# Kernel optimization log

Hardware: AMD Instinct MI355X
Metric: run time of the kernel (lower is better)

The kernel has to match this reference:

```python
import jax, jax.numpy as jnp
import numpy as np

B, S, C, H, D = 4, 2048, 512, 8, 64
EPS = 1e-5
SCALE = D ** -0.5


def layer_norm(x, w, b):
    m = jnp.mean(x, axis=-1, keepdims=True)
    v = jnp.var(x, axis=-1, keepdims=True)
    return (x - m) * jax.lax.rsqrt(v + EPS) * w + b


def setup_inputs() -> dict:
    key = jax.random.key(0)
    ks = jax.random.split(key, 7)
    s = 0.02
    return {
        "x": jax.random.normal(ks[0], (B, S, C), jnp.float32),
        "Wq": jax.random.normal(ks[1], (C, H * D), jnp.float32) * s,
        "Wk": jax.random.normal(ks[2], (C, H * D), jnp.float32) * s,
        "Wv": jax.random.normal(ks[3], (C, H * D), jnp.float32) * s,
        "Wo": jax.random.normal(ks[4], (H * D, C), jnp.float32) * s,
        "ln1_w": jnp.ones((C,), jnp.float32), "ln1_b": jnp.zeros((C,), jnp.float32),
        "ff_ln1_w": jnp.ones((C,), jnp.float32), "ff_ln1_b": jnp.zeros((C,), jnp.float32),
        "ff_w1": jax.random.normal(ks[5], (C, C), jnp.float32) * s, "ff_b1": jnp.zeros((C,), jnp.float32),
        "ff_ln2_w": jnp.ones((C,), jnp.float32), "ff_ln2_b": jnp.zeros((C,), jnp.float32),
        "ff_w2": jax.random.normal(ks[6], (C, C), jnp.float32) * s, "ff_b2": jnp.zeros((C,), jnp.float32),
        "ln2_w": jnp.ones((C,), jnp.float32), "ln2_b": jnp.zeros((C,), jnp.float32),
    }


def causal_attention(x, Wq, Wk, Wv, Wo):
    # Mathematically identical to the bucketed memory-efficient attention:
    # online-softmax bucketing changes compute order, not the result.
    q = (x @ Wq).reshape(B, S, H, D).transpose(0, 2, 1, 3)  # [B,H,S,D]
    k = (x @ Wk).reshape(B, S, H, D).transpose(0, 2, 1, 3)
    v = (x @ Wv).reshape(B, S, H, D).transpose(0, 2, 1, 3)
    scores = jnp.einsum('bhqd,bhkd->bhqk', q, k) * SCALE  # [B,H,S,S]
    causal = jnp.tril(jnp.ones((S, S), bool))
    scores = jnp.where(causal, scores, jnp.finfo(scores.dtype).min)
    attn = jax.nn.softmax(scores, axis=-1)
    out = jnp.einsum('bhqk,bhkd->bhqd', attn, v)
    out = out.transpose(0, 2, 1, 3).reshape(B, S, H * D)
    return out @ Wo


def reference(x, Wq, Wk, Wv, Wo, ln1_w, ln1_b, ff_ln1_w, ff_ln1_b, ff_w1, ff_b1,
              ff_ln2_w, ff_ln2_b, ff_w2, ff_b2, ln2_w, ln2_b):
    a = causal_attention(x, Wq, Wk, Wv, Wo)
    x_ln = layer_norm(a + x, ln1_w, ln1_b)
    h = layer_norm(x_ln, ff_ln1_w, ff_ln1_b) @ ff_w1 + ff_b1
    h = layer_norm(h, ff_ln2_w, ff_ln2_b) @ ff_w2 + ff_b2
    return layer_norm(h + x_ln, ln2_w, ln2_b)
```

## Files before the change

kernel.cpp:

```cpp
#include <hip/hip_runtime.h>

#define B_ 4
#define S_ 2048
#define C_ 512
#define H_ 8
#define D_ 64
#define M_ 8192

typedef short s8v __attribute__((ext_vector_type(8)));
typedef short s4v __attribute__((ext_vector_type(4)));
typedef float f4v __attribute__((ext_vector_type(4)));
typedef unsigned short u16;
typedef unsigned int u32;

__device__ __forceinline__ u16 f2b(float f) {
    u32 u = __builtin_bit_cast(u32, f);
    u = u + 0x7fffu + ((u >> 16) & 1u);
    return (u16)(u >> 16);
}

__device__ __forceinline__ void b2f8(const s8v v, float* f) {
    #pragma unroll
    for (int k = 0; k < 8; ++k)
        f[k] = __builtin_bit_cast(float, (u32)(u16)v[k] << 16);
}

__device__ __forceinline__ void gl2lds16(const void* g, void* l) {
    __builtin_amdgcn_global_load_lds(
        (const __attribute__((address_space(1))) void*)g,
        (__attribute__((address_space(3))) void*)l, 16, 0, 0);
}

__global__ __launch_bounds__(256) void prep_k(const float* __restrict__ x,
                                              u16* __restrict__ xb,
                                              const float* __restrict__ s0,
                                              const float* __restrict__ s1,
                                              const float* __restrict__ s2,
                                              const float* __restrict__ s3,
                                              const float* __restrict__ s4,
                                              const float* __restrict__ s5,
                                              u16* __restrict__ d0,
                                              u16* __restrict__ d1,
                                              u16* __restrict__ d2,
                                              u16* __restrict__ d3,
                                              u16* __restrict__ d4,
                                              u16* __restrict__ d5)
{
    __shared__ float t[32][33];
    const int bx = blockIdx.x;
    if (bx < 4096) {
        const int i = (bx * 256 + (int)threadIdx.x) * 4;
        const float4 v = *(const float4*)&x[i];
        ushort4 o;
        o.x = f2b(v.x); o.y = f2b(v.y); o.z = f2b(v.z); o.w = f2b(v.w);
        *(ushort4*)&xb[i] = o;
        return;
    }
    const int tb = bx - 4096;
    const int z = tb >> 8, rem = tb & 255;
    const float* W; u16* Wt;
    switch (z) {
        case 0: W = s0; Wt = d0; break;
        case 1: W = s1; Wt = d1; break;
        case 2: W = s2; Wt = d2; break;
        case 3: W = s3; Wt = d3; break;
        case 4: W = s4; Wt = d4; break;
        default: W = s5; Wt = d5; break;
    }
    const int tx = threadIdx.x & 31, ty = threadIdx.x >> 5;
    const int n0 = (rem & 15) * 32, k0 = (rem >> 4) * 32;
    #pragma unroll
    for (int i = 0; i < 4; ++i)
        t[ty + i * 8][tx] = W[(size_t)(k0 + ty + i * 8) * C_ + n0 + tx];
    __syncthreads();
    #pragma unroll
    for (int i = 0; i < 4; ++i)
        Wt[(size_t)(n0 + ty + i * 8) * C_ + k0 + tx] = f2b(t[tx][ty + i * 8]);
}

template <bool OB>
__global__ __launch_bounds__(256) void gemm_k(const u16* __restrict__ A,
                                              const u16* __restrict__ Bt,
                                              const float* __restrict__ bias,
                                              void* __restrict__ outv)
{
    __shared__ u16 As[2][4][16][32];
    __shared__ u16 Bs[2][4][16][32];
    const int tid = threadIdx.x;
    const int lane = tid & 63, w = tid >> 6;
    const int q4 = lane >> 4, l16 = lane & 15;
    const int wr = w >> 1, wc = w & 1;
    const int bm = blockIdx.y * 64, bn = blockIdx.x * 64;
    const int lr = lane >> 2, lc = (lane & 3) * 8;

    f4v acc[2][2];
    #pragma unroll
    for (int i = 0; i < 2; ++i)
        #pragma unroll
        for (int j = 0; j < 2; ++j) acc[i][j] = (f4v){0.f, 0.f, 0.f, 0.f};

    gl2lds16(A  + (size_t)(bm + w * 16 + lr) * C_ + lc, (char*)As + w * 1024);
    gl2lds16(Bt + (size_t)(bn + w * 16 + lr) * C_ + lc, (char*)Bs + w * 1024);

    for (int kt = 0; kt < 16; ++kt) {
        __syncthreads();
        const int buf = kt & 1;
        if (kt < 15) {
            const int nb = buf ^ 1, k0 = (kt + 1) * 32;
            gl2lds16(A  + (size_t)(bm + w * 16 + lr) * C_ + k0 + lc,
                     (char*)As + nb * 4096 + w * 1024);
            gl2lds16(Bt + (size_t)(bn + w * 16 + lr) * C_ + k0 + lc,
                     (char*)Bs + nb * 4096 + w * 1024);
        }
        s8v a[2], bfr[2];
        #pragma unroll
        for (int i = 0; i < 2; ++i) {
            const int row = wr * 32 + i * 16 + l16;
            a[i] = *(const s8v*)&As[buf][row >> 4][row & 15][q4 * 8];
        }
        #pragma unroll
        for (int j = 0; j < 2; ++j) {
            const int row = wc * 32 + j * 16 + l16;
            bfr[j] = *(const s8v*)&Bs[buf][row >> 4][row & 15][q4 * 8];
        }
        #pragma unroll
        for (int i = 0; i < 2; ++i)
            #pragma unroll
            for (int j = 0; j < 2; ++j)
                acc[i][j] = __builtin_amdgcn_mfma_f32_16x16x32_bf16(a[i], bfr[j], acc[i][j], 0, 0, 0);
    }

    #pragma unroll
    for (int j = 0; j < 2; ++j) {
        const int n = bn + wc * 32 + j * 16 + l16;
        const float bj = bias ? bias[n] : 0.0f;
        #pragma unroll
        for (int i = 0; i < 2; ++i) {
            const int m = bm + wr * 32 + i * 16 + q4 * 4;
            #pragma unroll
            for (int reg = 0; reg < 4; ++reg) {
                const float vv = acc[i][j][reg] + bj;
                if constexpr (OB) ((u16*)outv)[(size_t)(m + reg) * C_ + n] = f2b(vv);
                else              ((float*)outv)[(size_t)(m + reg) * C_ + n] = vv;
            }
        }
    }
}

__global__ __launch_bounds__(256) void qkv_k(const u16* __restrict__ A,
                                             const u16* __restrict__ Wq,
                                             const u16* __restrict__ Wk,
                                             const u16* __restrict__ Wv,
                                             u16* __restrict__ oq,
                                             u16* __restrict__ ok,
                                             u16* __restrict__ ovt)
{
    __shared__ u16 As[2][4][16][32];
    __shared__ u16 Bs[2][4][16][32];
    const int tid = threadIdx.x;
    const int lane = tid & 63, w = tid >> 6;
    const int q4 = lane >> 4, l16 = lane & 15;
    const int wr = w >> 1, wc = w & 1;
    const int nt = blockIdx.x, which = nt >> 3;
    const u16* Bt = which == 0 ? Wq : (which == 1 ? Wk : Wv);
    const int bm = blockIdx.y * 64, bn = (nt & 7) * 64;
    const int lr = lane >> 2, lc = (lane & 3) * 8;

    f4v acc[2][2];
    #pragma unroll
    for (int i = 0; i < 2; ++i)
        #pragma unroll
        for (int j = 0; j < 2; ++j) acc[i][j] = (f4v){0.f, 0.f, 0.f, 0.f};

    gl2lds16(A  + (size_t)(bm + w * 16 + lr) * C_ + lc, (char*)As + w * 1024);
    gl2lds16(Bt + (size_t)(bn + w * 16 + lr) * C_ + lc, (char*)Bs + w * 1024);

    for (int kt = 0; kt < 16; ++kt) {
        __syncthreads();
        const int buf = kt & 1;
        if (kt < 15) {
            const int nb = buf ^ 1, k0 = (kt + 1) * 32;
            gl2lds16(A  + (size_t)(bm + w * 16 + lr) * C_ + k0 + lc,
                     (char*)As + nb * 4096 + w * 1024);
            gl2lds16(Bt + (size_t)(bn + w * 16 + lr) * C_ + k0 + lc,
                     (char*)Bs + nb * 4096 + w * 1024);
        }
        s8v a[2], bfr[2];
        #pragma unroll
        for (int i = 0; i < 2; ++i) {
            const int row = wr * 32 + i * 16 + l16;
            a[i] = *(const s8v*)&As[buf][row >> 4][row & 15][q4 * 8];
        }
        #pragma unroll
        for (int j = 0; j < 2; ++j) {
            const int row = wc * 32 + j * 16 + l16;
            bfr[j] = *(const s8v*)&Bs[buf][row >> 4][row & 15][q4 * 8];
        }
        #pragma unroll
        for (int i = 0; i < 2; ++i)
            #pragma unroll
            for (int j = 0; j < 2; ++j)
                acc[i][j] = __builtin_amdgcn_mfma_f32_16x16x32_bf16(a[i], bfr[j], acc[i][j], 0, 0, 0);
    }

    if (which == 0) {
        #pragma unroll
        for (int j = 0; j < 2; ++j) {
            const int n = bn + wc * 32 + j * 16 + l16;
            #pragma unroll
            for (int i = 0; i < 2; ++i) {
                const int m = bm + wr * 32 + i * 16 + q4 * 4;
                #pragma unroll
                for (int reg = 0; reg < 4; ++reg)
                    oq[(size_t)(m + reg) * C_ + n] = f2b(acc[i][j][reg]);
            }
        }
    } else if (which == 1) {
        #pragma unroll
        for (int j = 0; j < 2; ++j) {
            const int n = bn + wc * 32 + j * 16 + l16;
            const int nswz = (n & ~31) | ((((n >> 3) & 3) ^ q4) << 3) | (n & 7);
            #pragma unroll
            for (int i = 0; i < 2; ++i) {
                const int m = bm + wr * 32 + i * 16 + q4 * 4;
                #pragma unroll
                for (int reg = 0; reg < 4; ++reg)
                    ok[(size_t)(m + reg) * C_ + nswz] = f2b(acc[i][j][reg]);
            }
        }
    } else {
        const int bglob = bm >> 11;
        const int sbase = bm & (S_ - 1);
        #pragma unroll
        for (int j = 0; j < 2; ++j) {
            const int n = bn + wc * 32 + j * 16 + l16;
            const int h = n >> 6, d = n & 63;
            u16* vrow = ovt + ((size_t)(bglob * H_ + h) * D_ + d) * S_;
            const int xw = d & 7;
            #pragma unroll
            for (int i = 0; i < 2; ++i) {
                const int s = sbase + wr * 32 + i * 16 + q4 * 4;
                const int pg = ((s & 31) >> 2) ^ xw;
                s4v pv;
                #pragma unroll
                for (int reg = 0; reg < 4; ++reg) pv[reg] = (short)f2b(acc[i][j][reg]);
                *(s4v*)&vrow[(s & ~31) + (pg << 2)] = pv;
            }
        }
    }
}

__global__ __launch_bounds__(256) void ln2xb_k(const u16* __restrict__ in,
                                               const float* __restrict__ res,
                                               const float* __restrict__ w1,
                                               const float* __restrict__ b1,
                                               const float* __restrict__ w2,
                                               const float* __restrict__ b2,
                                               u16* __restrict__ out1,
                                               u16* __restrict__ out2)
{
    const int lane = threadIdx.x & 63;
    const int row  = blockIdx.x * 4 + (threadIdx.x >> 6);
    const size_t off = (size_t)row * C_ + lane * 8;
    float v[8];
    b2f8(*(const s8v*)&in[off], v);
    {
        const float4 r0 = *(const float4*)&res[off];
        const float4 r1 = *(const float4*)&res[off + 4];
        v[0] += r0.x; v[1] += r0.y; v[2] += r0.z; v[3] += r0.w;
        v[4] += r1.x; v[5] += r1.y; v[6] += r1.z; v[7] += r1.w;
    }
    float s = 0.f, ss = 0.f;
    #pragma unroll
    for (int k = 0; k < 8; ++k) { s += v[k]; ss += v[k] * v[k]; }
    #pragma unroll
    for (int o = 32; o >= 1; o >>= 1) { s += __shfl_xor(s, o); ss += __shfl_xor(ss, o); }
    float mean = s * (1.0f / C_);
    float rstd = rsqrtf(ss * (1.0f / C_) - mean * mean + 1e-5f);

    const float4 wA0 = *(const float4*)&w1[lane * 8];
    const float4 wA1 = *(const float4*)&w1[lane * 8 + 4];
    const float4 bA0 = *(const float4*)&b1[lane * 8];
    const float4 bA1 = *(const float4*)&b1[lane * 8 + 4];
    const float wA[8] = {wA0.x, wA0.y, wA0.z, wA0.w, wA1.x, wA1.y, wA1.z, wA1.w};
    const float bA[8] = {bA0.x, bA0.y, bA0.z, bA0.w, bA1.x, bA1.y, bA1.z, bA1.w};
    float y[8];
    s8v o1;
    #pragma unroll
    for (int k = 0; k < 8; ++k) {
        y[k] = (v[k] - mean) * rstd * wA[k] + bA[k];
        o1[k] = (short)f2b(y[k]);
    }
    *(s8v*)&out1[off] = o1;

    s = 0.f; ss = 0.f;
    #pragma unroll
    for (int k = 0; k < 8; ++k) { s += y[k]; ss += y[k] * y[k]; }
    #pragma unroll
    for (int o = 32; o >= 1; o >>= 1) { s += __shfl_xor(s, o); ss += __shfl_xor(ss, o); }
    mean = s * (1.0f / C_);
    rstd = rsqrtf(ss * (1.0f / C_) - mean * mean + 1e-5f);

    const float4 wB0 = *(const float4*)&w2[lane * 8];
    const float4 wB1 = *(const float4*)&w2[lane * 8 + 4];
    const float4 bB0 = *(const float4*)&b2[lane * 8];
    const float4 bB1 = *(const float4*)&b2[lane * 8 + 4];
    const float wB[8] = {wB0.x, wB0.y, wB0.z, wB0.w, wB1.x, wB1.y, wB1.z, wB1.w};
    const float bB[8] = {bB0.x, bB0.y, bB0.z, bB0.w, bB1.x, bB1.y, bB1.z, bB1.w};
    s8v o2;
    #pragma unroll
    for (int k = 0; k < 8; ++k)
        o2[k] = (short)f2b((y[k] - mean) * rstd * wB[k] + bB[k]);
    *(s8v*)&out2[off] = o2;
}

__global__ __launch_bounds__(256) void lnb_k(const u16* __restrict__ in,
                                             const float* __restrict__ w,
                                             const float* __restrict__ bb,
                                             u16* __restrict__ out)
{
    const int lane = threadIdx.x & 63;
    const int row  = blockIdx.x * 4 + (threadIdx.x >> 6);
    const size_t off = (size_t)row * C_ + lane * 8;
    float v[8];
    b2f8(*(const s8v*)&in[off], v);
    float s = 0.f, ss = 0.f;
    #pragma unroll
    for (int k = 0; k < 8; ++k) { s += v[k]; ss += v[k] * v[k]; }
    #pragma unroll
    for (int o = 32; o >= 1; o >>= 1) { s += __shfl_xor(s, o); ss += __shfl_xor(ss, o); }
    const float mean = s * (1.0f / C_);
    const float rstd = rsqrtf(ss * (1.0f / C_) - mean * mean + 1e-5f);
    const float4 w0 = *(const float4*)&w[lane * 8];
    const float4 w1 = *(const float4*)&w[lane * 8 + 4];
    const float4 b0 = *(const float4*)&bb[lane * 8];
    const float4 b1 = *(const float4*)&bb[lane * 8 + 4];
    const float wv[8] = {w0.x, w0.y, w0.z, w0.w, w1.x, w1.y, w1.z, w1.w};
    const float bv[8] = {b0.x, b0.y, b0.z, b0.w, b1.x, b1.y, b1.z, b1.w};
    s8v o;
    #pragma unroll
    for (int k = 0; k < 8; ++k)
        o[k] = (short)f2b((v[k] - mean) * rstd * wv[k] + bv[k]);
    *(s8v*)&out[off] = o;
}

__global__ __launch_bounds__(256) void lnfin_k(const u16* __restrict__ in,
                                               const u16* __restrict__ res,
                                               const float* __restrict__ w,
                                               const float* __restrict__ bb,
                                               float* __restrict__ out)
{
    const int lane = threadIdx.x & 63;
    const int row  = blockIdx.x * 4 + (threadIdx.x >> 6);
    const size_t off = (size_t)row * C_ + lane * 8;
    float v[8], r[8];
    b2f8(*(const s8v*)&in[off], v);
    b2f8(*(const s8v*)&res[off], r);
    #pragma unroll
    for (int k = 0; k < 8; ++k) v[k] += r[k];
    float s = 0.f, ss = 0.f;
    #pragma unroll
    for (int k = 0; k < 8; ++k) { s += v[k]; ss += v[k] * v[k]; }
    #pragma unroll
    for (int o = 32; o >= 1; o >>= 1) { s += __shfl_xor(s, o); ss += __shfl_xor(ss, o); }
    const float mean = s * (1.0f / C_);
    const float rstd = rsqrtf(ss * (1.0f / C_) - mean * mean + 1e-5f);
    const float4 w0 = *(const float4*)&w[lane * 8];
    const float4 w1 = *(const float4*)&w[lane * 8 + 4];
    const float4 b0 = *(const float4*)&bb[lane * 8];
    const float4 b1 = *(const float4*)&bb[lane * 8 + 4];
    const float wv[8] = {w0.x, w0.y, w0.z, w0.w, w1.x, w1.y, w1.z, w1.w};
    const float bv[8] = {b0.x, b0.y, b0.z, b0.w, b1.x, b1.y, b1.z, b1.w};
    float4 o0, o1;
    o0.x = (v[0] - mean) * rstd * wv[0] + bv[0];
    o0.y = (v[1] - mean) * rstd * wv[1] + bv[1];
    o0.z = (v[2] - mean) * rstd * wv[2] + bv[2];
    o0.w = (v[3] - mean) * rstd * wv[3] + bv[3];
    o1.x = (v[4] - mean) * rstd * wv[4] + bv[4];
    o1.y = (v[5] - mean) * rstd * wv[5] + bv[5];
    o1.z = (v[6] - mean) * rstd * wv[6] + bv[6];
    o1.w = (v[7] - mean) * rstd * wv[7] + bv[7];
    *(float4*)&out[off]     = o0;
    *(float4*)&out[off + 4] = o1;
}

__global__ __launch_bounds__(256) void attn_k(const u16* __restrict__ Q,
                                              const u16* __restrict__ K,
                                              const u16* __restrict__ Vt,
                                              u16* __restrict__ O)
{
    __shared__ u16 Ks[2][2][64][32];
    __shared__ u16 Vs[2][2][64][32];
    const int tid = threadIdx.x;
    const int lane = tid & 63, w = tid >> 6;
    const int q4 = lane >> 4, l16 = lane & 15;
    const int h = blockIdx.y, b = blockIdx.z;
    const int qb = 31 - (int)blockIdx.x;
    const size_t base  = ((size_t)b * S_) * C_ + h * D_;
    const size_t basev = ((size_t)(b * H_ + h)) * D_ * S_;
    const int lr = lane >> 2, lc = (lane & 3) * 8;
    const int kq = (q4 ^ ((l16 >> 2) & 3)) * 8;

    s8v qf[2];
    #pragma unroll
    for (int kh = 0; kh < 2; ++kh)
        qf[kh] = *(const s8v*)&Q[base + (size_t)(qb * 64 + w * 16 + l16) * C_ + kh * 32 + q4 * 8];

    #pragma unroll
    for (int r = 0; r < 2; ++r) {
        const int seg = r * 4 + w;
        const int row = (seg & 3) * 16 + lr;
        const int kh = seg >> 2;
        gl2lds16(K  + base  + (size_t)row * C_ + kh * 32 + lc, (char*)Ks + seg * 1024);
        gl2lds16(Vt + basev + (size_t)row * S_ + kh * 32 + lc, (char*)Vs + seg * 1024);
    }

    f4v o[4];
    float lp[4] = {0.f, 0.f, 0.f, 0.f};
    #pragma unroll
    for (int j = 0; j < 4; ++j) o[j] = (f4v){0.f, 0.f, 0.f, 0.f};

    const int qrow = w * 16 + l16;
    for (int kb = 0; kb <= qb; ++kb) {
        __syncthreads();
        const int buf = kb & 1;
        if (kb < qb) {
            const int nb = buf ^ 1, kn = kb + 1;
            #pragma unroll
            for (int r = 0; r < 2; ++r) {
                const int seg = r * 4 + w;
                const int row = (seg & 3) * 16 + lr;
                const int kh = seg >> 2;
                gl2lds16(K  + base  + (size_t)(kn * 64 + row) * C_ + kh * 32 + lc,
                         (char*)Ks + nb * 8192 + seg * 1024);
                gl2lds16(Vt + basev + (size_t)row * S_ + kn * 64 + kh * 32 + lc,
                         (char*)Vs + nb * 8192 + seg * 1024);
            }
        }

        f4v sc[4];
        #pragma unroll
        for (int j = 0; j < 4; ++j) sc[j] = (f4v){0.f, 0.f, 0.f, 0.f};
        #pragma unroll
        for (int kh = 0; kh < 2; ++kh) {
            #pragma unroll
            for (int j = 0; j < 4; ++j) {
                const s8v kf = *(const s8v*)&Ks[buf][kh][j * 16 + l16][kq];
                sc[j] = __builtin_amdgcn_mfma_f32_16x16x32_bf16(kf, qf[kh], sc[j], 0, 0, 0);
            }
        }

        s4v pa[4];
        if (kb == qb) {
            #pragma unroll
            for (int j = 0; j < 4; ++j) {
                float ps = 0.0f;
                #pragma unroll
                for (int reg = 0; reg < 4; ++reg) {
                    float t = fmaf(sc[j][reg], 0.18033688011112043f, -11.541560327111707f);
                    if ((j * 16 + q4 * 4 + reg) > qrow) t = -128.0f;
                    const float p = exp2f(t);
                    ps += p;
                    pa[j][reg] = (short)(__builtin_bit_cast(u32, p) >> 16);
                }
                lp[j] += ps;
            }
        } else {
            #pragma unroll
            for (int j = 0; j < 4; ++j) {
                float ps = 0.0f;
                #pragma unroll
                for (int reg = 0; reg < 4; ++reg) {
                    const float p = exp2f(fmaf(sc[j][reg], 0.18033688011112043f,
                                               -11.541560327111707f));
                    ps += p;
                    pa[j][reg] = (short)(__builtin_bit_cast(u32, p) >> 16);
                }
                lp[j] += ps;
            }
        }

        #pragma unroll
        for (int c = 0; c < 4; ++c) {
            const int gh = (((c & 1) * 4 + q4) ^ (l16 & 7)) * 4;
            #pragma unroll
            for (int dj = 0; dj < 4; ++dj) {
                const s4v vb = *(const s4v*)&Vs[buf][c >> 1][dj * 16 + l16][gh];
                o[dj] = __builtin_amdgcn_mfma_f32_16x16x16bf16_1k(pa[c], vb, o[dj], 0, 0, 0);
            }
        }
    }

    float lt = (lp[0] + lp[1]) + (lp[2] + lp[3]);
    lt += __shfl_xor(lt, 16);
    lt += __shfl_xor(lt, 32);
    #pragma unroll
    for (int reg = 0; reg < 4; ++reg) {
        const float inv = 1.0f / __shfl(lt, q4 * 4 + reg);
        const size_t rowoff = base + (size_t)(qb * 64 + w * 16 + q4 * 4 + reg) * C_;
        #pragma unroll
        for (int dj = 0; dj < 4; ++dj)
            O[rowoff + dj * 16 + l16] = f2b(o[dj][reg] * inv);
    }
}

extern "C" void kernel_launch(void* const* d_in, const int* in_sizes, int n_in,
                              void* d_out, int out_size, void* d_ws, size_t ws_size,
                              hipStream_t stream)
{
    const float* x       = (const float*)d_in[0];
    const float* Wq      = (const float*)d_in[1];
    const float* Wk      = (const float*)d_in[2];
    const float* Wv      = (const float*)d_in[3];
    const float* Wo      = (const float*)d_in[4];
    const float* ln1_w   = (const float*)d_in[5];
    const float* ln1_b   = (const float*)d_in[6];
    const float* ffln1_w = (const float*)d_in[7];
    const float* ffln1_b = (const float*)d_in[8];
    const float* ff_w1   = (const float*)d_in[9];
    const float* ff_b1   = (const float*)d_in[10];
    const float* ffln2_w = (const float*)d_in[11];
    const float* ffln2_b = (const float*)d_in[12];
    const float* ff_w2   = (const float*)d_in[13];
    const float* ff_b2   = (const float*)d_in[14];
    const float* ln2_w   = (const float*)d_in[15];
    const float* ln2_b   = (const float*)d_in[16];
    float* out = (float*)d_out;

    const size_t MC = (size_t)M_ * C_;
    const size_t WW = (size_t)C_ * C_;
    u16* xb   = (u16*)d_ws;
    u16* WqT  = xb + MC;
    u16* WkT  = WqT + WW;
    u16* WvT  = WkT + WW;
    u16* WoT  = WvT + WW;
    u16* W1T  = WoT + WW;
    u16* W2T  = W1T + WW;
    u16* qbuf = W2T + WW;
    u16* kbuf = qbuf + MC;
    u16* vbuf = kbuf + MC;
    u16* vtbuf= vbuf + MC;
    u16*  abuf = xb;
    u16*  tf   = qbuf;
    u16*  xln  = vbuf;

    const dim3 gg(C_ / 64, M_ / 64);
    const dim3 gq(24, M_ / 64);
    const dim3 ga(32, H_, B_);
    const int  gl = M_ / 4;

    prep_k<<<5632, 256, 0, stream>>>(x, xb, Wq, Wk, Wv, Wo, ff_w1, ff_w2,
                                     WqT, WkT, WvT, WoT, W1T, W2T);

    qkv_k<<<gq, 256, 0, stream>>>(xb, WqT, WkT, WvT, qbuf, kbuf, vtbuf);
    attn_k<<<ga, 256, 0, stream>>>(qbuf, kbuf, vtbuf, abuf);

    gemm_k<true><<<gg, 256, 0, stream>>>(abuf, WoT, nullptr, tf);
    ln2xb_k<<<gl, 256, 0, stream>>>(tf, x, ln1_w, ln1_b, ffln1_w, ffln1_b,
                                    xln, xb);
    gemm_k<true><<<gg, 256, 0, stream>>>(xb, W1T, ff_b1, tf);
    lnb_k<<<gl, 256, 0, stream>>>(tf, ffln2_w, ffln2_b, xb);
    gemm_k<true><<<gg, 256, 0, stream>>>(xb, W2T, ff_b2, tf);
    lnfin_k<<<gl, 256, 0, stream>>>(tf, xln, ln2_w, ln2_b, out);
}
```

Before: 262.7 us.

## Enlarge GEMM tiles to 128x64 with K=64 stages and XOR-swizzled LDS

Both the generic GEMM and the fused QKV projection now use 128x64 output tiles with 64-wide K stages instead of 64x64 tiles with 32-wide K stages. Each wave computes a 64x32 sub-tile (4x2 MFMAs) and does two MFMA k-steps per barrier. The LDS layout is row-major with an XOR swizzle to avoid bank conflicts. The grid is transposed so consecutive blocks walk along M and share the same weight tile. This cuts the number of barriers and global loads per MFMA, at the cost of more LDS and registers per block and fewer blocks overall.

Result: faster. 242.7 us (-7.6%).

```diff
diff --git a/kernel.cpp b/kernel.cpp
--- a/kernel.cpp
+++ b/kernel.cpp
@@ -84,50 +84,58 @@
                                               const float* __restrict__ bias,
                                               void* __restrict__ outv)
 {
-    __shared__ u16 As[2][4][16][32];
-    __shared__ u16 Bs[2][4][16][32];
+    __shared__ u16 As[2][128][64];
+    __shared__ u16 Bs[2][64][64];
     const int tid = threadIdx.x;
     const int lane = tid & 63, w = tid >> 6;
     const int q4 = lane >> 4, l16 = lane & 15;
     const int wr = w >> 1, wc = w & 1;
-    const int bm = blockIdx.y * 64, bn = blockIdx.x * 64;
-    const int lr = lane >> 2, lc = (lane & 3) * 8;
-
-    f4v acc[2][2];
-    #pragma unroll
-    for (int i = 0; i < 2; ++i)
+    const int bm = blockIdx.x * 128, bn = blockIdx.y * 64;
+    const int sr8  = lane >> 3;
+    const int scol = ((lane & 7) ^ sr8) * 8;
+
+    f4v acc[4][2];
+    #pragma unroll
+    for (int i = 0; i < 4; ++i)
         #pragma unroll
         for (int j = 0; j < 2; ++j) acc[i][j] = (f4v){0.f, 0.f, 0.f, 0.f};
 
-    gl2lds16(A  + (size_t)(bm + w * 16 + lr) * C_ + lc, (char*)As + w * 1024);
-    gl2lds16(Bt + (size_t)(bn + w * 16 + lr) * C_ + lc, (char*)Bs + w * 1024);
-
-    for (int kt = 0; kt < 16; ++kt) {
+    const u16* Ab = A  + (size_t)bm * C_;
+    const u16* Bb = Bt + (size_t)bn * C_;
+
+    auto stage = [&](int bf, int kt) {
+        const int k0 = kt * 64;
+        #pragma unroll
+        for (int t = 0; t < 4; ++t)
+            gl2lds16(Ab + (size_t)(w * 32 + t * 8 + sr8) * C_ + k0 + scol,
+                     (char*)As + bf * 16384 + (w * 32 + t * 8) * 128);
+        #pragma unroll
+        for (int t = 0; t < 2; ++t)
+            gl2lds16(Bb + (size_t)(w * 16 + t * 8 + sr8) * C_ + k0 + scol,
+                     (char*)Bs + bf * 8192 + (w * 16 + t * 8) * 128);
+    };
+
+    stage(0, 0);
+    for (int kt = 0; kt < 8; ++kt) {
         __syncthreads();
-        const int buf = kt & 1;
-        if (kt < 15) {
-            const int nb = buf ^ 1, k0 = (kt + 1) * 32;
-            gl2lds16(A  + (size_t)(bm + w * 16 + lr) * C_ + k0 + lc,
-                     (char*)As + nb * 4096 + w * 1024);
-            gl2lds16(Bt + (size_t)(bn + w * 16 + lr) * C_ + k0 + lc,
-                     (char*)Bs + nb * 4096 + w * 1024);
-        }
-        s8v a[2], bfr[2];
-        #pragma unroll
-        for (int i = 0; i < 2; ++i) {
-            const int row = wr * 32 + i * 16 + l16;
-            a[i] = *(const s8v*)&As[buf][row >> 4][row & 15][q4 * 8];
-        }
-        #pragma unroll
-        for (int j = 0; j < 2; ++j) {
-            const int row = wc * 32 + j * 16 + l16;
-            bfr[j] = *(const s8v*)&Bs[buf][row >> 4][row & 15][q4 * 8];
-        }
-        #pragma unroll
-        for (int i = 0; i < 2; ++i)
+        const int bf = kt & 1;
+        if (kt < 7) stage(bf ^ 1, kt + 1);
+        #pragma unroll
+        for (int kk = 0; kk < 2; ++kk) {
+            const int pc = ((kk * 4 + q4) ^ (l16 & 7)) * 8;
+            s8v a[4], b[2];
+            #pragma unroll
+            for (int i = 0; i < 4; ++i)
+                a[i] = *(const s8v*)&As[bf][wr * 64 + i * 16 + l16][pc];
             #pragma unroll
             for (int j = 0; j < 2; ++j)
-                acc[i][j] = __builtin_amdgcn_mfma_f32_16x16x32_bf16(a[i], bfr[j], acc[i][j], 0, 0, 0);
+                b[j] = *(const s8v*)&Bs[bf][wc * 32 + j * 16 + l16][pc];
+            #pragma unroll
+            for (int i = 0; i < 4; ++i)
+                #pragma unroll
+                for (int j = 0; j < 2; ++j)
+                    acc[i][j] = __builtin_amdgcn_mfma_f32_16x16x32_bf16(a[i], b[j], acc[i][j], 0, 0, 0);
+        }
     }
 
     #pragma unroll
@@ -135,8 +143,8 @@
         const int n = bn + wc * 32 + j * 16 + l16;
         const float bj = bias ? bias[n] : 0.0f;
         #pragma unroll
-        for (int i = 0; i < 2; ++i) {
-            const int m = bm + wr * 32 + i * 16 + q4 * 4;
+        for (int i = 0; i < 4; ++i) {
+            const int m = bm + wr * 64 + i * 16 + q4 * 4;
             #pragma unroll
             for (int reg = 0; reg < 4; ++reg) {
                 const float vv = acc[i][j][reg] + bj;
@@ -155,52 +163,60 @@
                                              u16* __restrict__ ok,
                                              u16* __restrict__ ovt)
 {
-    __shared__ u16 As[2][4][16][32];
-    __shared__ u16 Bs[2][4][16][32];
+    __shared__ u16 As[2][128][64];
+    __shared__ u16 Bs[2][64][64];
     const int tid = threadIdx.x;
     const int lane = tid & 63, w = tid >> 6;
     const int q4 = lane >> 4, l16 = lane & 15;
     const int wr = w >> 1, wc = w & 1;
-    const int nt = blockIdx.x, which = nt >> 3;
+    const int nt = blockIdx.y, which = nt >> 3;
     const u16* Bt = which == 0 ? Wq : (which == 1 ? Wk : Wv);
-    const int bm = blockIdx.y * 64, bn = (nt & 7) * 64;
-    const int lr = lane >> 2, lc = (lane & 3) * 8;
-
-    f4v acc[2][2];
-    #pragma unroll
-    for (int i = 0; i < 2; ++i)
+    const int bm = blockIdx.x * 128, bn = (nt & 7) * 64;
+    const int sr8  = lane >> 3;
+    const int scol = ((lane & 7) ^ sr8) * 8;
+
+    f4v acc[4][2];
+    #pragma unroll
+    for (int i = 0; i < 4; ++i)
         #pragma unroll
         for (int j = 0; j < 2; ++j) acc[i][j] = (f4v){0.f, 0.f, 0.f, 0.f};
 
-    gl2lds16(A  + (size_t)(bm + w * 16 + lr) * C_ + lc, (char*)As + w * 1024);
-    gl2lds16(Bt + (size_t)(bn + w * 16 + lr) * C_ + lc, (char*)Bs + w * 1024);
-
-    for (int kt = 0; kt < 16; ++kt) {
+    const u16* Ab = A  + (size_t)bm * C_;
+    const u16* Bb = Bt + (size_t)bn * C_;
+
+    auto stage = [&](int bf, int kt) {
+        const int k0 = kt * 64;
+        #pragma unroll
+        for (int t = 0; t < 4; ++t)
+            gl2lds16(Ab + (size_t)(w * 32 + t * 8 + sr8) * C_ + k0 + scol,
+                     (char*)As + bf * 16384 + (w * 32 + t * 8) * 128);
+        #pragma unroll
+        for (int t = 0; t < 2; ++t)
+            gl2lds16(Bb + (size_t)(w * 16 + t * 8 + sr8) * C_ + k0 + scol,
+                     (char*)Bs + bf * 8192 + (w * 16 + t * 8) * 128);
+    };
+
+    stage(0, 0);
+    for (int kt = 0; kt < 8; ++kt) {
         __syncthreads();
-        const int buf = kt & 1;
-        if (kt < 15) {
-            const int nb = buf ^ 1, k0 = (kt + 1) * 32;
-            gl2lds16(A  + (size_t)(bm + w * 16 + lr) * C_ + k0 + lc,
-                     (char*)As + nb * 4096 + w * 1024);
-            gl2lds16(Bt + (size_t)(bn + w * 16 + lr) * C_ + k0 + lc,
-                     (char*)Bs + nb * 4096 + w * 1024);
-        }
-        s8v a[2], bfr[2];
-        #pragma unroll
-        for (int i = 0; i < 2; ++i) {
-            const int row = wr * 32 + i * 16 + l16;
-            a[i] = *(const s8v*)&As[buf][row >> 4][row & 15][q4 * 8];
-        }
-        #pragma unroll
-        for (int j = 0; j < 2; ++j) {
-            const int row = wc * 32 + j * 16 + l16;
-            bfr[j] = *(const s8v*)&Bs[buf][row >> 4][row & 15][q4 * 8];
-        }
-        #pragma unroll
-        for (int i = 0; i < 2; ++i)
+        const int bf = kt & 1;
+        if (kt < 7) stage(bf ^ 1, kt + 1);
+        #pragma unroll
+        for (int kk = 0; kk < 2; ++kk) {
+            const int pc = ((kk * 4 + q4) ^ (l16 & 7)) * 8;
+            s8v a[4], b[2];
+            #pragma unroll
+            for (int i = 0; i < 4; ++i)
+                a[i] = *(const s8v*)&As[bf][wr * 64 + i * 16 + l16][pc];
             #pragma unroll
             for (int j = 0; j < 2; ++j)
-                acc[i][j] = __builtin_amdgcn_mfma_f32_16x16x32_bf16(a[i], bfr[j], acc[i][j], 0, 0, 0);
+                b[j] = *(const s8v*)&Bs[bf][wc * 32 + j * 16 + l16][pc];
+            #pragma unroll
+            for (int i = 0; i < 4; ++i)
+                #pragma unroll
+                for (int j = 0; j < 2; ++j)
+                    acc[i][j] = __builtin_amdgcn_mfma_f32_16x16x32_bf16(a[i], b[j], acc[i][j], 0, 0, 0);
+        }
     }
 
     if (which == 0) {
@@ -208,8 +224,8 @@
         for (int j = 0; j < 2; ++j) {
             const int n = bn + wc * 32 + j * 16 + l16;
             #pragma unroll
-            for (int i = 0; i < 2; ++i) {
-                const int m = bm + wr * 32 + i * 16 + q4 * 4;
+            for (int i = 0; i < 4; ++i) {
+                const int m = bm + wr * 64 + i * 16 + q4 * 4;
                 #pragma unroll
                 for (int reg = 0; reg < 4; ++reg)
                     oq[(size_t)(m + reg) * C_ + n] = f2b(acc[i][j][reg]);
@@ -221,8 +237,8 @@
             const int n = bn + wc * 32 + j * 16 + l16;
             const int nswz = (n & ~31) | ((((n >> 3) & 3) ^ q4) << 3) | (n & 7);
             #pragma unroll
-            for (int i = 0; i < 2; ++i) {
-                const int m = bm + wr * 32 + i * 16 + q4 * 4;
+            for (int i = 0; i < 4; ++i) {
+                const int m = bm + wr * 64 + i * 16 + q4 * 4;
                 #pragma unroll
                 for (int reg = 0; reg < 4; ++reg)
                     ok[(size_t)(m + reg) * C_ + nswz] = f2b(acc[i][j][reg]);
@@ -238,8 +254,8 @@
             u16* vrow = ovt + ((size_t)(bglob * H_ + h) * D_ + d) * S_;
             const int xw = d & 7;
             #pragma unroll
-            for (int i = 0; i < 2; ++i) {
-                const int s = sbase + wr * 32 + i * 16 + q4 * 4;
+            for (int i = 0; i < 4; ++i) {
+                const int s = sbase + wr * 64 + i * 16 + q4 * 4;
                 const int pg = ((s & 31) >> 2) ^ xw;
                 s4v pv;
                 #pragma unroll
@@ -544,8 +560,8 @@
     u16*  tf   = qbuf;
     u16*  xln  = vbuf;
 
-    const dim3 gg(C_ / 64, M_ / 64);
-    const dim3 gq(24, M_ / 64);
+    const dim3 gg(M_ / 128, C_ / 64);
+    const dim3 gq(M_ / 128, 24);
     const dim3 ga(32, H_, B_);
     const int  gl = M_ / 4;
 
```
